# Kernel optimization log

Measured on AMD Instinct MI355X. Metric: run time of the kernel, lower is better.

The kernel has to match this reference:

```python
import jax, jax.numpy as jnp
import numpy as np

N, E, D = 10000, 640000, 128
H1, H2, OUT = 256, 256, 64
EPS = 1e-5

def _layernorm(h, g, b):
    m = jnp.mean(h, axis=-1, keepdims=True)
    v = jnp.mean((h - m) ** 2, axis=-1, keepdims=True)
    return (h - m) * jax.lax.rsqrt(v + EPS) * g + b

def setup_inputs() -> dict:
    key = jax.random.key(0)
    ks = jax.random.split(key, 20)
    def lin(k, fan_in, fan_out):
        bound = 1.0 / np.sqrt(fan_in)
        kw, kb = jax.random.split(k)
        W = jax.random.uniform(kw, (fan_in, fan_out), jnp.float32, -bound, bound)
        b = jax.random.uniform(kb, (fan_out,), jnp.float32, -bound, bound)
        return W, b
    pool_w, pool_b = lin(ks[0], D, D)
    w1, b1 = lin(ks[1], D, H1)
    w2, b2 = lin(ks[2], H1, H2)
    mu_w, mu_b = lin(ks[3], H2, OUT)
    lv_w, lv_b = lin(ks[4], H2, OUT)
    return {
        "x": jax.random.normal(ks[5], (N, D), jnp.float32),
        "edge_index": jax.random.randint(ks[6], (2, E), 0, N, jnp.int32),
        "edge_strength": jax.random.uniform(ks[7], (E,), jnp.float32),
        "ewmc": jnp.float32(0.5),
        "pool_w": pool_w, "pool_b": pool_b,
        "lnp_g": jnp.ones((D,), jnp.float32), "lnp_b": jnp.zeros((D,), jnp.float32),
        "w1": w1, "b1": b1,
        "ln1_g": jnp.ones((H1,), jnp.float32), "ln1_b": jnp.zeros((H1,), jnp.float32),
        "w2": w2, "b2": b2,
        "ln2_g": jnp.ones((H2,), jnp.float32), "ln2_b": jnp.zeros((H2,), jnp.float32),
        "mu_w": mu_w, "mu_b": mu_b,
        "lv_w": lv_w, "lv_b": lv_b,
    }

def reference(x, edge_index, edge_strength, ewmc, pool_w, pool_b, lnp_g, lnp_b,
              w1, b1, ln1_g, ln1_b, w2, b2, ln2_g, ln2_b, mu_w, mu_b, lv_w, lv_b):
    src, dst = edge_index[0], edge_index[1]
    coef = jax.nn.softplus(ewmc)
    # [E, D] gather + edge scaling
    msgs = x[src] * (1.0 + coef * edge_strength[:, None])
    pooled = jax.nn.relu(_layernorm(msgs @ pool_w + pool_b, lnp_g, lnp_b))
    # segment max by dst; torch_scatter fills empty segments with 0 and pooled >= 0
    agg = jax.ops.segment_max(pooled, dst, num_segments=x.shape[0])
    agg = jnp.maximum(agg, 0.0)
    h = jax.nn.relu(_layernorm(agg @ w1 + b1, ln1_g, ln1_b))
    h = jax.nn.relu(_layernorm(h @ w2 + b2, ln2_g, ln2_b))
    mu = h @ mu_w + mu_b
    logvar = h @ lv_w + lv_b
    std = jnp.exp(0.5 * logvar)
    return (mu, std)
```

## Files before the change

### kernel.cpp

```cpp
#include <hip/hip_runtime.h>
#include <math.h>

#define D_DIM   128
#define H1_DIM  256
#define H2_DIM  256
#define OUT_DIM 64
#define LN_EPS  1e-5f
#define NSHARD  4
#define AGGP_STRIDE 2048

typedef __attribute__((ext_vector_type(8))) short bf16x8;
typedef __attribute__((ext_vector_type(4))) float f32x4;

__device__ __forceinline__ unsigned short bf16rne(float v) {
    unsigned int b = __float_as_uint(v);
    return (unsigned short)((b + 0x7FFFu + ((b >> 16) & 1u)) >> 16);
}

union BFPack { unsigned int u[4]; bf16x8 v; };

__global__ __launch_bounds__(512) void k_pool(
        const float* __restrict__ x, const float* __restrict__ pw,
        const float* __restrict__ pb,
        unsigned short* __restrict__ y, float4* __restrict__ stat4,
        const int* __restrict__ ei, int* __restrict__ cnt, int E, int epb,
        const float* __restrict__ w1, const float* __restrict__ w2,
        const float* __restrict__ muw, const float* __restrict__ lvw,
        short* __restrict__ wp1, short* __restrict__ wp2,
        short* __restrict__ wpH) {
    __shared__ __align__(16) short aPack[4 * 64 * 8];
    __shared__ unsigned short yLds[16][128];
    __shared__ float sPart[16][8][3];
    const int tid  = threadIdx.x;
    const int w    = tid >> 6;
    const int lane = tid & 63;
    const int gq   = lane >> 4;
    const int c16  = lane & 15;
    const int row0 = blockIdx.x * 16;

    bf16x8 bfrag[4];
    {
        const int col = w * 16 + c16;
        const int kbase = gq * 8;
#pragma unroll
        for (int kt = 0; kt < 4; ++kt) {
            int k0 = kt * 32 + kbase;
            BFPack t;
#pragma unroll
            for (int jj = 0; jj < 4; ++jj) {
                float a = pw[(k0 + 2 * jj) * D_DIM + col];
                float b = pw[(k0 + 2 * jj + 1) * D_DIM + col];
                t.u[jj] = (unsigned int)bf16rne(a) | ((unsigned int)bf16rne(b) << 16);
            }
            bfrag[kt] = t.v;
        }
    }
    {
        int ebeg = blockIdx.x * epb;
        int eend = ebeg + epb; if (eend > E) eend = E;
        for (int e = ebeg + tid; e < eend; e += 512)
            atomicAdd(&cnt[ei[E + e] * NSHARD + (e & (NSHARD - 1))], 1);
    }
    {
        int r  = tid >> 5;
        int k0 = (tid & 31) * 4;
        float4 v = *(const float4*)&x[(size_t)(row0 + r) * D_DIM + k0];
        int kt = k0 >> 5, sub = (k0 >> 3) & 3, j = k0 & 7;
        int lp = r | (sub << 4);
        unsigned int u0 = (unsigned int)bf16rne(v.x) | ((unsigned int)bf16rne(v.y) << 16);
        unsigned int u1 = (unsigned int)bf16rne(v.z) | ((unsigned int)bf16rne(v.w) << 16);
        *(uint2*)&aPack[kt * 512 + lp * 8 + j] = make_uint2(u0, u1);
    }
    __syncthreads();

    f32x4 A = {0.f, 0.f, 0.f, 0.f};
#pragma unroll
    for (int kt = 0; kt < 4; ++kt) {
        bf16x8 av = *(bf16x8*)&aPack[(kt * 64 + lane) * 8];
        A = __builtin_amdgcn_mfma_f32_16x16x32_bf16(av, bfrag[kt], A, 0, 0, 0);
    }

    {
        float pbf = pb[w * 16 + c16];
#pragma unroll
        for (int r = 0; r < 4; ++r) {
            unsigned short h = bf16rne(A[r]);
            yLds[gq * 4 + r][w * 16 + c16] = h;
            float hf = __uint_as_float((unsigned int)h << 16);
            float s1 = hf, s2 = hf * hf, s3 = hf * pbf;
#pragma unroll
            for (int m = 1; m < 16; m <<= 1) {
                s1 += __shfl_xor(s1, m, 64);
                s2 += __shfl_xor(s2, m, 64);
                s3 += __shfl_xor(s3, m, 64);
            }
            if (c16 == 0) {
                sPart[gq * 4 + r][w][0] = s1;
                sPart[gq * 4 + r][w][1] = s2;
                sPart[gq * 4 + r][w][2] = s3;
            }
        }
    }
    __syncthreads();
    {
        int idx = tid * 4;
        int r = idx >> 7, c = idx & 127;
        *(uint2*)&y[(size_t)(row0 + r) * D_DIM + c] = *(const uint2*)&yLds[r][c];
    }
    if (tid < 16) {
        float t1 = 0.f, t2 = 0.f, t3 = 0.f;
#pragma unroll
        for (int ww = 0; ww < 8; ++ww) {
            t1 += sPart[tid][ww][0]; t2 += sPart[tid][ww][1]; t3 += sPart[tid][ww][2];
        }
        stat4[row0 + tid] = make_float4(t1 * (1.f / 128.f), t2 * (1.f / 128.f),
                                        t3 * (1.f / 128.f), 0.f);
    }
    if (blockIdx.x < 32) {
        int i = blockIdx.x * 512 + tid;
        const float* W; int Ndim, kt, ln, col; short* dst;
        if (i < 4096) {
            int q = i >> 6; ln = i & 63; kt = q & 3; int ct = q >> 2;
            W = w1; Ndim = H1_DIM; col = ct * 16 + (ln & 15); dst = wp1 + i * 8;
        } else if (i < 12288) {
            int i2 = i - 4096; int q = i2 >> 6; ln = i2 & 63; kt = q & 7; int ct = q >> 3;
            W = w2; Ndim = H2_DIM; col = ct * 16 + (ln & 15); dst = wp2 + i2 * 8;
        } else {
            int i3 = i - 12288; int q = i3 >> 6; ln = i3 & 63; kt = q & 7; int ct = q >> 3;
            Ndim = OUT_DIM; dst = wpH + i3 * 8;
            if (ct < 4) { W = muw; col = ct * 16 + (ln & 15); }
            else        { W = lvw; col = (ct - 4) * 16 + (ln & 15); }
        }
        int k0 = kt * 32 + (ln >> 4) * 8;
        unsigned int u[4];
#pragma unroll
        for (int jj = 0; jj < 4; ++jj) {
            float a = W[(k0 + 2 * jj) * Ndim + col];
            float b = W[(k0 + 2 * jj + 1) * Ndim + col];
            u[jj] = (unsigned int)bf16rne(a) | ((unsigned int)bf16rne(b) << 16);
        }
        *(uint4*)dst = make_uint4(u[0], u[1], u[2], u[3]);
    }
}

__global__ __launch_bounds__(1024) void k_scanA(
        const int* __restrict__ cnt, int* __restrict__ offs,
        int* __restrict__ bsum, int N4) {
    __shared__ int part[1024];
    const int t = threadIdx.x;
    const int idx = blockIdx.x * 1024 + t;
    int v = (idx < N4) ? cnt[idx] : 0;
    part[t] = v;
    __syncthreads();
    for (int off = 1; off < 1024; off <<= 1) {
        int n = (t >= off) ? part[t - off] : 0;
        __syncthreads();
        part[t] += n;
        __syncthreads();
    }
    if (idx < N4) offs[idx] = part[t] - v;
    if (t == 1023) bsum[blockIdx.x] = part[t];
}

__global__ __launch_bounds__(64) void k_scanB(
        const int* __restrict__ bsum, int* __restrict__ bbase,
        int* __restrict__ offs, float* __restrict__ consts,
        const float* __restrict__ ewmc, const float* __restrict__ pb,
        int nblk, int N4) {
    const int l = threadIdx.x;
    {
        float v0 = pb[l], v1 = pb[l + 64];
        float s1 = v0 + v1, s2 = v0 * v0 + v1 * v1;
#pragma unroll
        for (int off = 1; off < 64; off <<= 1) {
            s1 += __shfl_xor(s1, off, 64);
            s2 += __shfl_xor(s2, off, 64);
        }
        if (l == 0) {
            float xw = ewmc[0];
            consts[0] = (xw > 30.f) ? xw : log1pf(expf(xw));
            consts[1] = s1 * (1.f / 128.f);
            consts[2] = s2 * (1.f / 128.f);
        }
    }
    int val = (l < nblk) ? bsum[l] : 0;
    int orig = val;
#pragma unroll
    for (int off = 1; off < 64; off <<= 1) {
        int n = __shfl_up(val, off, 64);
        if (l >= off) val += n;
    }
    if (l < nblk) bbase[l] = val - orig;
    if (l == nblk - 1) offs[N4] = val;
}

__global__ __launch_bounds__(1024) void k_scanC(
        int* __restrict__ offs, int* __restrict__ head,
        const int* __restrict__ bbase, int N4) {
    int idx = blockIdx.x * 1024 + threadIdx.x;
    if (idx < N4) {
        int o = offs[idx] + bbase[blockIdx.x];
        offs[idx] = o;
        head[idx] = o;
    }
}

__global__ __launch_bounds__(256) void k_scatter(
        const int* __restrict__ ei, const float* __restrict__ es,
        const float* __restrict__ consts, const float4* __restrict__ stat4,
        int* __restrict__ head, float4* __restrict__ pairs, int E) {
    const float coef = consts[0], mpb = consts[1], mpb2 = consts[2];
    const int tid = threadIdx.x;
    const int e0 = blockIdx.x * 2048 + tid;
    int srcv[8], dstv[8]; float sv[8]; float4 st[8]; int pos[8]; bool ok[8];
#pragma unroll
    for (int u = 0; u < 8; ++u) {
        int e = e0 + u * 256;
        ok[u] = (e < E);
        if (ok[u]) { srcv[u] = ei[e]; dstv[u] = ei[E + e]; sv[u] = es[e]; }
    }
#pragma unroll
    for (int u = 0; u < 8; ++u) if (ok[u]) st[u] = stat4[srcv[u]];
#pragma unroll
    for (int u = 0; u < 8; ++u) if (ok[u]) {
        int e = e0 + u * 256;
        pos[u] = atomicAdd(&head[dstv[u] * NSHARD + (e & (NSHARD - 1))], 1);
    }
#pragma unroll
    for (int u = 0; u < 8; ++u) if (ok[u]) {
        float s = fmaf(coef, sv[u], 1.0f);
        float m   = fmaf(s, st[u].x, mpb);
        float et2 = fmaf(s * s, st[u].y, fmaf(2.f * s, st[u].z, mpb2));
        float inv = rsqrtf(et2 - m * m + LN_EPS);
        pairs[pos[u]] = make_float4(__int_as_float(srcv[u]), s, m, inv);
    }
}

#define GPROC(P, YB)                                                          \
    {                                                                         \
        float s = (P).y, m = (P).z, inv = (P).w;                              \
        float y0 = __uint_as_float((YB).x << 16);                             \
        float y1 = __uint_as_float((YB).x & 0xFFFF0000u);                     \
        float y2 = __uint_as_float((YB).y << 16);                             \
        float y3 = __uint_as_float((YB).y & 0xFFFF0000u);                     \
        float y4 = __uint_as_float((YB).z << 16);                             \
        float y5 = __uint_as_float((YB).z & 0xFFFF0000u);                     \
        float y6 = __uint_as_float((YB).w << 16);                             \
        float y7 = __uint_as_float((YB).w & 0xFFFF0000u);                     \
        mxA.x = fmaxf(mxA.x, fmaf(fmaf(s, y0, pbA.x) - m, inv * gA.x, bA.x)); \
        mxA.y = fmaxf(mxA.y, fmaf(fmaf(s, y1, pbA.y) - m, inv * gA.y, bA.y)); \
        mxA.z = fmaxf(mxA.z, fmaf(fmaf(s, y2, pbA.z) - m, inv * gA.z, bA.z)); \
        mxA.w = fmaxf(mxA.w, fmaf(fmaf(s, y3, pbA.w) - m, inv * gA.w, bA.w)); \
        mxB.x = fmaxf(mxB.x, fmaf(fmaf(s, y4, pbB.x) - m, inv * gB.x, bB.x)); \
        mxB.y = fmaxf(mxB.y, fmaf(fmaf(s, y5, pbB.y) - m, inv * gB.y, bB.y)); \
        mxB.z = fmaxf(mxB.z, fmaf(fmaf(s, y6, pbB.z) - m, inv * gB.z, bB.z)); \
        mxB.w = fmaxf(mxB.w, fmaf(fmaf(s, y7, pbB.w) - m, inv * gB.w, bB.w)); \
    }

__global__ __launch_bounds__(256) void k_gather(
        const float4* __restrict__ pairs, const int* __restrict__ offs,
        const unsigned short* __restrict__ y, const float* __restrict__ pb,
        const float* __restrict__ g, const float* __restrict__ b,
        unsigned short* __restrict__ aggP, int N) {
    const int node = blockIdx.x * 4 + (threadIdx.x >> 6);
    if (node >= N) return;
    const int lane = threadIdx.x & 63;
    const int sub  = lane >> 4;
    const int q    = lane & 15;
    const int d0   = q * 8;
    const float4 pbA = *(const float4*)&pb[d0], pbB = *(const float4*)&pb[d0 + 4];
    const float4 gA  = *(const float4*)&g[d0],  gB  = *(const float4*)&g[d0 + 4];
    const float4 bA  = *(const float4*)&b[d0],  bB  = *(const float4*)&b[d0 + 4];
    float4 mxA = make_float4(-INFINITY, -INFINITY, -INFINITY, -INFINITY);
    float4 mxB = mxA;
    int j = offs[node * NSHARD];
    const int end = offs[node * NSHARD + NSHARD];
    for (; j + 12 <= end; j += 12) {
        float4 p[3]; uint4 yb[3];
#pragma unroll
        for (int u = 0; u < 3; ++u) p[u] = pairs[j + 4 * u + sub];
#pragma unroll
        for (int u = 0; u < 3; ++u)
            yb[u] = *(const uint4*)&y[(size_t)__float_as_int(p[u].x) * D_DIM + d0];
#pragma unroll
        for (int u = 0; u < 3; ++u) GPROC(p[u], yb[u]);
    }
    for (; j + 4 <= end; j += 4) {
        float4 p = pairs[j + sub];
        uint4 yb = *(const uint4*)&y[(size_t)__float_as_int(p.x) * D_DIM + d0];
        GPROC(p, yb);
    }
    if (j < end) {
        int rem = end - j;
        float4 p = pairs[j + (sub < rem ? sub : 0)];
        uint4 yb = *(const uint4*)&y[(size_t)__float_as_int(p.x) * D_DIM + d0];
        GPROC(p, yb);
    }
    mxA.x = fmaxf(mxA.x, __shfl_xor(mxA.x, 16, 64));
    mxA.y = fmaxf(mxA.y, __shfl_xor(mxA.y, 16, 64));
    mxA.z = fmaxf(mxA.z, __shfl_xor(mxA.z, 16, 64));
    mxA.w = fmaxf(mxA.w, __shfl_xor(mxA.w, 16, 64));
    mxB.x = fmaxf(mxB.x, __shfl_xor(mxB.x, 16, 64));
    mxB.y = fmaxf(mxB.y, __shfl_xor(mxB.y, 16, 64));
    mxB.z = fmaxf(mxB.z, __shfl_xor(mxB.z, 16, 64));
    mxB.w = fmaxf(mxB.w, __shfl_xor(mxB.w, 16, 64));
    mxA.x = fmaxf(mxA.x, __shfl_xor(mxA.x, 32, 64));
    mxA.y = fmaxf(mxA.y, __shfl_xor(mxA.y, 32, 64));
    mxA.z = fmaxf(mxA.z, __shfl_xor(mxA.z, 32, 64));
    mxA.w = fmaxf(mxA.w, __shfl_xor(mxA.w, 32, 64));
    mxB.x = fmaxf(mxB.x, __shfl_xor(mxB.x, 32, 64));
    mxB.y = fmaxf(mxB.y, __shfl_xor(mxB.y, 32, 64));
    mxB.z = fmaxf(mxB.z, __shfl_xor(mxB.z, 32, 64));
    mxB.w = fmaxf(mxB.w, __shfl_xor(mxB.w, 32, 64));
    if (sub == 0) {
        unsigned int u0 = (unsigned int)bf16rne(fmaxf(mxA.x, 0.f))
                        | ((unsigned int)bf16rne(fmaxf(mxA.y, 0.f)) << 16);
        unsigned int u1 = (unsigned int)bf16rne(fmaxf(mxA.z, 0.f))
                        | ((unsigned int)bf16rne(fmaxf(mxA.w, 0.f)) << 16);
        unsigned int u2 = (unsigned int)bf16rne(fmaxf(mxB.x, 0.f))
                        | ((unsigned int)bf16rne(fmaxf(mxB.y, 0.f)) << 16);
        unsigned int u3 = (unsigned int)bf16rne(fmaxf(mxB.z, 0.f))
                        | ((unsigned int)bf16rne(fmaxf(mxB.w, 0.f)) << 16);
        int kt = q >> 2, sfr = q & 3, lp = (node & 15) | (sfr << 4);
        *(uint4*)&aggP[(size_t)(node >> 4) * AGGP_STRIDE + kt * 512 + lp * 8] =
            make_uint4(u0, u1, u2, u3);
    }
}

__global__ __launch_bounds__(512) void k_mlp(
        const unsigned short* __restrict__ aggP,
        const short* __restrict__ wp1, const short* __restrict__ wp2,
        const short* __restrict__ wpH,
        const float* __restrict__ b1, const float* __restrict__ g1,
        const float* __restrict__ bb1,
        const float* __restrict__ b2, const float* __restrict__ g2,
        const float* __restrict__ bb2,
        const float* __restrict__ mub, const float* __restrict__ lvb,
        float* __restrict__ out, int N) {
    __shared__ __align__(16) short aPack[8 * 64 * 8];
    __shared__ float sPart[16][8][2];
    __shared__ float sM[16], sI[16];
    const int tid  = threadIdx.x;
    const int w    = tid >> 6;
    const int lane = tid & 63;
    const int gq   = lane >> 4;
    const int c16  = lane & 15;
    const int row0 = blockIdx.x * 16;
    const unsigned short* aG = aggP + (size_t)blockIdx.x * AGGP_STRIDE;

    const int ct0 = 2 * w, ct1 = 2 * w + 1;
    f32x4 A0 = {0.f, 0.f, 0.f, 0.f}, A1 = {0.f, 0.f, 0.f, 0.f};

#pragma unroll
    for (int kt = 0; kt < 4; ++kt) {
        bf16x8 av = *(const bf16x8*)&aG[(kt * 64 + lane) * 8];
        bf16x8 bv0 = *(const bf16x8*)&wp1[((ct0 * 4 + kt) * 64 + lane) * 8];
        bf16x8 bv1 = *(const bf16x8*)&wp1[((ct1 * 4 + kt) * 64 + lane) * 8];
        A0 = __builtin_amdgcn_mfma_f32_16x16x32_bf16(av, bv0, A0, 0, 0, 0);
        A1 = __builtin_amdgcn_mfma_f32_16x16x32_bf16(av, bv1, A1, 0, 0, 0);
    }
    {
        int col0 = ct0 * 16 + c16, col1 = ct1 * 16 + c16;
        float bias0 = b1[col0], bias1 = b1[col1];
        float v0[4], v1[4];
#pragma unroll
        for (int r = 0; r < 4; ++r) {
            v0[r] = A0[r] + bias0; v1[r] = A1[r] + bias1;
            float s1 = v0[r] + v1[r];
            float s2 = v0[r] * v0[r] + v1[r] * v1[r];
#pragma unroll
            for (int m = 1; m < 16; m <<= 1) {
                s1 += __shfl_xor(s1, m, 64);
                s2 += __shfl_xor(s2, m, 64);
            }
            if (c16 == 0) { sPart[gq * 4 + r][w][0] = s1; sPart[gq * 4 + r][w][1] = s2; }
        }
        __syncthreads();
        if (tid < 16) {
            float t1 = 0.f, t2 = 0.f;
#pragma unroll
            for (int ww = 0; ww < 8; ++ww) { t1 += sPart[tid][ww][0]; t2 += sPart[tid][ww][1]; }
            float m = t1 * (1.f / 256.f);
            sM[tid] = m;
            sI[tid] = rsqrtf(t2 * (1.f / 256.f) - m * m + LN_EPS);
        }
        __syncthreads();
        float gc0 = g1[col0], bc0 = bb1[col0];
        float gc1 = g1[col1], bc1 = bb1[col1];
#pragma unroll
        for (int r = 0; r < 4; ++r) {
            int row = gq * 4 + r;
            float m = sM[row], inv = sI[row];
            float h0 = fmaxf(fmaf((v0[r] - m) * inv, gc0, bc0), 0.f);
            float h1 = fmaxf(fmaf((v1[r] - m) * inv, gc1, bc1), 0.f);
            aPack[(col0 >> 5) * 512 + (row | (((col0 >> 3) & 3) << 4)) * 8 + (col0 & 7)] = (short)bf16rne(h0);
            aPack[(col1 >> 5) * 512 + (row | (((col1 >> 3) & 3) << 4)) * 8 + (col1 & 7)] = (short)bf16rne(h1);
        }
    }
    __syncthreads();

    A0 = (f32x4){0.f, 0.f, 0.f, 0.f}; A1 = (f32x4){0.f, 0.f, 0.f, 0.f};
#pragma unroll
    for (int kt = 0; kt < 8; ++kt) {
        bf16x8 av = *(bf16x8*)&aPack[(kt * 64 + lane) * 8];
        bf16x8 bv0 = *(const bf16x8*)&wp2[((ct0 * 8 + kt) * 64 + lane) * 8];
        bf16x8 bv1 = *(const bf16x8*)&wp2[((ct1 * 8 + kt) * 64 + lane) * 8];
        A0 = __builtin_amdgcn_mfma_f32_16x16x32_bf16(av, bv0, A0, 0, 0, 0);
        A1 = __builtin_amdgcn_mfma_f32_16x16x32_bf16(av, bv1, A1, 0, 0, 0);
    }
    {
        int col0 = ct0 * 16 + c16, col1 = ct1 * 16 + c16;
        float bias0 = b2[col0], bias1 = b2[col1];
        float v0[4], v1[4];
#pragma unroll
        for (int r = 0; r < 4; ++r) {
            v0[r] = A0[r] + bias0; v1[r] = A1[r] + bias1;
            float s1 = v0[r] + v1[r];
            float s2 = v0[r] * v0[r] + v1[r] * v1[r];
#pragma unroll
            for (int m = 1; m < 16; m <<= 1) {
                s1 += __shfl_xor(s1, m, 64);
                s2 += __shfl_xor(s2, m, 64);
            }
            if (c16 == 0) { sPart[gq * 4 + r][w][0] = s1; sPart[gq * 4 + r][w][1] = s2; }
        }
        __syncthreads();
        if (tid < 16) {
            float t1 = 0.f, t2 = 0.f;
#pragma unroll
            for (int ww = 0; ww < 8; ++ww) { t1 += sPart[tid][ww][0]; t2 += sPart[tid][ww][1]; }
            float m = t1 * (1.f / 256.f);
            sM[tid] = m;
            sI[tid] = rsqrtf(t2 * (1.f / 256.f) - m * m + LN_EPS);
        }
        __syncthreads();
        float gc0 = g2[col0], bc0 = bb2[col0];
        float gc1 = g2[col1], bc1 = bb2[col1];
#pragma unroll
        for (int r = 0; r < 4; ++r) {
            int row = gq * 4 + r;
            float m = sM[row], inv = sI[row];
            float h0 = fmaxf(fmaf((v0[r] - m) * inv, gc0, bc0), 0.f);
            float h1 = fmaxf(fmaf((v1[r] - m) * inv, gc1, bc1), 0.f);
            aPack[(col0 >> 5) * 512 + (row | (((col0 >> 3) & 3) << 4)) * 8 + (col0 & 7)] = (short)bf16rne(h0);
            aPack[(col1 >> 5) * 512 + (row | (((col1 >> 3) & 3) << 4)) * 8 + (col1 & 7)] = (short)bf16rne(h1);
        }
    }
    __syncthreads();

    {
        f32x4 H = {0.f, 0.f, 0.f, 0.f};
#pragma unroll
        for (int kt = 0; kt < 8; ++kt) {
            bf16x8 av = *(bf16x8*)&aPack[(kt * 64 + lane) * 8];
            bf16x8 bv = *(const bf16x8*)&wpH[((w * 8 + kt) * 64 + lane) * 8];
            H = __builtin_amdgcn_mfma_f32_16x16x32_bf16(av, bv, H, 0, 0, 0);
        }
        int colh = (w & 3) * 16 + c16;
        if (w < 4) {
            float bias = mub[colh];
#pragma unroll
            for (int r = 0; r < 4; ++r)
                out[(size_t)(row0 + gq * 4 + r) * OUT_DIM + colh] = H[r] + bias;
        } else {
            float bias = lvb[colh];
#pragma unroll
            for (int r = 0; r < 4; ++r)
                out[(size_t)N * OUT_DIM + (size_t)(row0 + gq * 4 + r) * OUT_DIM + colh] =
                    expf(0.5f * (H[r] + bias));
        }
    }
}

extern "C" void kernel_launch(void* const* d_in, const int* in_sizes, int n_in,
                              void* d_out, int out_size, void* d_ws, size_t ws_size,
                              hipStream_t stream) {
    const float* x      = (const float*)d_in[0];
    const int*   ei     = (const int*)  d_in[1];
    const float* es     = (const float*)d_in[2];
    const float* ewmc   = (const float*)d_in[3];
    const float* pool_w = (const float*)d_in[4];
    const float* pool_b = (const float*)d_in[5];
    const float* lnp_g  = (const float*)d_in[6];
    const float* lnp_b  = (const float*)d_in[7];
    const float* w1     = (const float*)d_in[8];
    const float* b1     = (const float*)d_in[9];
    const float* ln1_g  = (const float*)d_in[10];
    const float* ln1_b  = (const float*)d_in[11];
    const float* w2     = (const float*)d_in[12];
    const float* b2     = (const float*)d_in[13];
    const float* ln2_g  = (const float*)d_in[14];
    const float* ln2_b  = (const float*)d_in[15];
    const float* mu_w   = (const float*)d_in[16];
    const float* mu_b   = (const float*)d_in[17];
    const float* lv_w   = (const float*)d_in[18];
    const float* lv_b   = (const float*)d_in[19];

    const int N  = in_sizes[0] / D_DIM;
    const int E  = in_sizes[2];
    const int N4 = N * NSHARD;
    const int nblkScan = (N4 + 1023) / 1024;

    float*  ws     = (float*)d_ws;
    float*  consts = ws;
    float4* stat4  = (float4*)(ws + 16);
    unsigned short* y    = (unsigned short*)(ws + 16 + 4 * (size_t)N);
    unsigned short* aggP = y + (size_t)N * D_DIM;
    size_t  w      = 16 + 4 * (size_t)N + (size_t)N * D_DIM;
    int*    cnt    = (int*)(ws + w); w += N4;
    int*    offs   = (int*)(ws + w); w += N4 + 1;
    int*    head   = (int*)(ws + w); w += N4;
    int*    bsum   = (int*)(ws + w); w += 64;
    int*    bbase  = (int*)(ws + w); w += 64;
    w = (w + 3) & ~(size_t)3;
    short*  wp1    = (short*)(ws + w); w += 16384;
    short*  wp2    = (short*)(ws + w); w += 32768;
    short*  wpH    = (short*)(ws + w); w += 16384;
    float4* pairs  = (float4*)(ws + w);

    const int nbPool = N / 16;
    const int epb    = (E + nbPool - 1) / nbPool;

    hipMemsetAsync(cnt, 0, (size_t)N4 * sizeof(int), stream);
    k_pool<<<nbPool, 512, 0, stream>>>(x, pool_w, pool_b, y, stat4, ei, cnt, E,
                                       epb, w1, w2, mu_w, lv_w, wp1, wp2, wpH);
    k_scanA<<<nblkScan, 1024, 0, stream>>>(cnt, offs, bsum, N4);
    k_scanB<<<1, 64, 0, stream>>>(bsum, bbase, offs, consts, ewmc, pool_b,
                                  nblkScan, N4);
    k_scanC<<<nblkScan, 1024, 0, stream>>>(offs, head, bbase, N4);
    k_scatter<<<(E + 2047) / 2048, 256, 0, stream>>>(ei, es, consts, stat4,
                                                     head, pairs, E);
    k_gather<<<(N + 3) / 4, 256, 0, stream>>>(pairs, offs, y,
                                              pool_b, lnp_g, lnp_b, aggP, N);
    k_mlp<<<N / 16, 512, 0, stream>>>(aggP, wp1, wp2, wpH,
                                      b1, ln1_g, ln1_b,
                                      b2, ln2_g, ln2_b,
                                      mu_b, lv_b, (float*)d_out, N);
}
```

Baseline: 116.5 us.

## Fold scan fix-up kernels into scatter and gather via per-block base recompute

Removes the k_scanB and k_scanC launches. Each scatter and gather block now rebuilds the 64-entry block-base prefix in shared memory from bsum and adds it to the local offsets on the fly. The scatter atomics now run on a zeroed head0 counter array, cleared by the enlarged memset, instead of a copied head. Scatter edges per block drop from 8 to 4 per thread, and the gather unroll grows from 3 to 4. This saves two launches and a pass over the offsets, at the cost of a redundant small prefix scan in every block plus an extra offsL load per edge.

```diff
diff --git a/kernel.cpp b/kernel.cpp
--- a/kernel.cpp
+++ b/kernel.cpp
@@ -144,8 +144,25 @@
 }
 
 __global__ __launch_bounds__(1024) void k_scanA(
-        const int* __restrict__ cnt, int* __restrict__ offs,
-        int* __restrict__ bsum, int N4) {
+        const int* __restrict__ cnt, int* __restrict__ offsL,
+        int* __restrict__ bsum, float* __restrict__ consts,
+        const float* __restrict__ ewmc, const float* __restrict__ pb, int N4) {
+    if (blockIdx.x == 0 && threadIdx.x < 64) {
+        const int l = threadIdx.x;
+        float v0 = pb[l], v1 = pb[l + 64];
+        float s1 = v0 + v1, s2 = v0 * v0 + v1 * v1;
+#pragma unroll
+        for (int off = 1; off < 64; off <<= 1) {
+            s1 += __shfl_xor(s1, off, 64);
+            s2 += __shfl_xor(s2, off, 64);
+        }
+        if (l == 0) {
+            float xw = ewmc[0];
+            consts[0] = (xw > 30.f) ? xw : log1pf(expf(xw));
+            consts[1] = s1 * (1.f / 128.f);
+            consts[2] = s2 * (1.f / 128.f);
+        }
+    }
     __shared__ int part[1024];
     const int t = threadIdx.x;
     const int idx = blockIdx.x * 1024 + t;
@@ -158,81 +175,66 @@
         part[t] += n;
         __syncthreads();
     }
-    if (idx < N4) offs[idx] = part[t] - v;
+    if (idx < N4) offsL[idx] = part[t] - v;
     if (t == 1023) bsum[blockIdx.x] = part[t];
 }
 
-__global__ __launch_bounds__(64) void k_scanB(
-        const int* __restrict__ bsum, int* __restrict__ bbase,
-        int* __restrict__ offs, float* __restrict__ consts,
-        const float* __restrict__ ewmc, const float* __restrict__ pb,
-        int nblk, int N4) {
-    const int l = threadIdx.x;
-    {
-        float v0 = pb[l], v1 = pb[l + 64];
-        float s1 = v0 + v1, s2 = v0 * v0 + v1 * v1;
+__device__ __forceinline__ void build_bb(const int* __restrict__ bsum,
+                                         int* bbL, int* totalL,
+                                         int tid, int nblk) {
+    if (tid < 64) {
+        int v = (tid < nblk) ? bsum[tid] : 0;
+        int val = v;
 #pragma unroll
         for (int off = 1; off < 64; off <<= 1) {
-            s1 += __shfl_xor(s1, off, 64);
-            s2 += __shfl_xor(s2, off, 64);
-        }
-        if (l == 0) {
-            float xw = ewmc[0];
-            consts[0] = (xw > 30.f) ? xw : log1pf(expf(xw));
-            consts[1] = s1 * (1.f / 128.f);
-            consts[2] = s2 * (1.f / 128.f);
-        }
-    }
-    int val = (l < nblk) ? bsum[l] : 0;
-    int orig = val;
-#pragma unroll
-    for (int off = 1; off < 64; off <<= 1) {
-        int n = __shfl_up(val, off, 64);
-        if (l >= off) val += n;
-    }
-    if (l < nblk) bbase[l] = val - orig;
-    if (l == nblk - 1) offs[N4] = val;
-}
-
-__global__ __launch_bounds__(1024) void k_scanC(
-        int* __restrict__ offs, int* __restrict__ head,
-        const int* __restrict__ bbase, int N4) {
-    int idx = blockIdx.x * 1024 + threadIdx.x;
-    if (idx < N4) {
-        int o = offs[idx] + bbase[blockIdx.x];
-        offs[idx] = o;
-        head[idx] = o;
+            int n = __shfl_up(val, off, 64);
+            if (tid >= off) val += n;
+        }
+        if (tid < nblk) bbL[tid] = val - v;
+        if (tid == nblk - 1) *totalL = val;
     }
 }
 
 __global__ __launch_bounds__(256) void k_scatter(
         const int* __restrict__ ei, const float* __restrict__ es,
         const float* __restrict__ consts, const float4* __restrict__ stat4,
-        int* __restrict__ head, float4* __restrict__ pairs, int E) {
+        int* __restrict__ head0, const int* __restrict__ offsL,
+        const int* __restrict__ bsum, float4* __restrict__ pairs,
+        int E, int nblk) {
+    __shared__ int bbL[64];
+    __shared__ int totalL;
+    const int tid = threadIdx.x;
+    build_bb(bsum, bbL, &totalL, tid, nblk);
+    __syncthreads();
     const float coef = consts[0], mpb = consts[1], mpb2 = consts[2];
-    const int tid = threadIdx.x;
-    const int e0 = blockIdx.x * 2048 + tid;
-    int srcv[8], dstv[8]; float sv[8]; float4 st[8]; int pos[8]; bool ok[8];
-#pragma unroll
-    for (int u = 0; u < 8; ++u) {
+    const int e0 = blockIdx.x * 1024 + tid;
+    int srcv[4], idxv[4]; float sv[4]; float4 st[4]; int base[4], pos[4];
+    bool ok[4];
+#pragma unroll
+    for (int u = 0; u < 4; ++u) {
         int e = e0 + u * 256;
         ok[u] = (e < E);
-        if (ok[u]) { srcv[u] = ei[e]; dstv[u] = ei[E + e]; sv[u] = es[e]; }
-    }
-#pragma unroll
-    for (int u = 0; u < 8; ++u) if (ok[u]) st[u] = stat4[srcv[u]];
-#pragma unroll
-    for (int u = 0; u < 8; ++u) if (ok[u]) {
-        int e = e0 + u * 256;
-        pos[u] = atomicAdd(&head[dstv[u] * NSHARD + (e & (NSHARD - 1))], 1);
-    }
-#pragma unroll
-    for (int u = 0; u < 8; ++u) if (ok[u]) {
+        if (ok[u]) {
+            srcv[u] = ei[e];
+            idxv[u] = ei[E + e] * NSHARD + (e & (NSHARD - 1));
+            sv[u] = es[e];
+        }
+    }
+#pragma unroll
+    for (int u = 0; u < 4; ++u) if (ok[u]) {
+        st[u] = stat4[srcv[u]];
+        base[u] = offsL[idxv[u]] + bbL[idxv[u] >> 10];
+    }
+#pragma unroll
+    for (int u = 0; u < 4; ++u) if (ok[u])
+        pos[u] = atomicAdd(&head0[idxv[u]], 1);
+#pragma unroll
+    for (int u = 0; u < 4; ++u) if (ok[u]) {
         float s = fmaf(coef, sv[u], 1.0f);
         float m   = fmaf(s, st[u].x, mpb);
         float et2 = fmaf(s * s, st[u].y, fmaf(2.f * s, st[u].z, mpb2));
         float inv = rsqrtf(et2 - m * m + LN_EPS);
-        pairs[pos[u]] = make_float4(__int_as_float(srcv[u]), s, m, inv);
+        pairs[base[u] + pos[u]] = make_float4(__int_as_float(srcv[u]), s, m, inv);
     }
 }
 
@@ -258,13 +260,19 @@
     }
 
 __global__ __launch_bounds__(256) void k_gather(
-        const float4* __restrict__ pairs, const int* __restrict__ offs,
+        const float4* __restrict__ pairs, const int* __restrict__ offsL,
+        const int* __restrict__ bsum,
         const unsigned short* __restrict__ y, const float* __restrict__ pb,
         const float* __restrict__ g, const float* __restrict__ b,
-        unsigned short* __restrict__ aggP, int N) {
-    const int node = blockIdx.x * 4 + (threadIdx.x >> 6);
+        unsigned short* __restrict__ aggP, int N, int N4, int nblk) {
+    __shared__ int bbL[64];
+    __shared__ int totalL;
+    const int tid = threadIdx.x;
+    build_bb(bsum, bbL, &totalL, tid, nblk);
+    __syncthreads();
+    const int node = blockIdx.x * 4 + (tid >> 6);
     if (node >= N) return;
-    const int lane = threadIdx.x & 63;
+    const int lane = tid & 63;
     const int sub  = lane >> 4;
     const int q    = lane & 15;
     const int d0   = q * 8;
@@ -273,17 +281,19 @@
     const float4 bA  = *(const float4*)&b[d0],  bB  = *(const float4*)&b[d0 + 4];
     float4 mxA = make_float4(-INFINITY, -INFINITY, -INFINITY, -INFINITY);
     float4 mxB = mxA;
-    int j = offs[node * NSHARD];
-    const int end = offs[node * NSHARD + NSHARD];
-    for (; j + 12 <= end; j += 12) {
-        float4 p[3]; uint4 yb[3];
-#pragma unroll
-        for (int u = 0; u < 3; ++u) p[u] = pairs[j + 4 * u + sub];
-#pragma unroll
-        for (int u = 0; u < 3; ++u)
+    const int idx0 = node * NSHARD;
+    const int idxe = idx0 + NSHARD;
+    int j = offsL[idx0] + bbL[idx0 >> 10];
+    const int end = (idxe < N4) ? (offsL[idxe] + bbL[idxe >> 10]) : totalL;
+    for (; j + 16 <= end; j += 16) {
+        float4 p[4]; uint4 yb[4];
+#pragma unroll
+        for (int u = 0; u < 4; ++u) p[u] = pairs[j + 4 * u + sub];
+#pragma unroll
+        for (int u = 0; u < 4; ++u)
             yb[u] = *(const uint4*)&y[(size_t)__float_as_int(p[u].x) * D_DIM + d0];
 #pragma unroll
-        for (int u = 0; u < 3; ++u) GPROC(p[u], yb[u]);
+        for (int u = 0; u < 4; ++u) GPROC(p[u], yb[u]);
     }
     for (; j + 4 <= end; j += 4) {
         float4 p = pairs[j + sub];
@@ -508,10 +518,9 @@
     unsigned short* aggP = y + (size_t)N * D_DIM;
     size_t  w      = 16 + 4 * (size_t)N + (size_t)N * D_DIM;
     int*    cnt    = (int*)(ws + w); w += N4;
-    int*    offs   = (int*)(ws + w); w += N4 + 1;
-    int*    head   = (int*)(ws + w); w += N4;
+    int*    head0  = (int*)(ws + w); w += N4;
+    int*    offsL  = (int*)(ws + w); w += N4;
     int*    bsum   = (int*)(ws + w); w += 64;
-    int*    bbase  = (int*)(ws + w); w += 64;
     w = (w + 3) & ~(size_t)3;
     short*  wp1    = (short*)(ws + w); w += 16384;
     short*  wp2    = (short*)(ws + w); w += 32768;
@@ -521,17 +530,17 @@
     const int nbPool = N / 16;
     const int epb    = (E + nbPool - 1) / nbPool;
 
-    hipMemsetAsync(cnt, 0, (size_t)N4 * sizeof(int), stream);
+    hipMemsetAsync(cnt, 0, 2 * (size_t)N4 * sizeof(int), stream);
     k_pool<<<nbPool, 512, 0, stream>>>(x, pool_w, pool_b, y, stat4, ei, cnt, E,
                                        epb, w1, w2, mu_w, lv_w, wp1, wp2, wpH);
-    k_scanA<<<nblkScan, 1024, 0, stream>>>(cnt, offs, bsum, N4);
-    k_scanB<<<1, 64, 0, stream>>>(bsum, bbase, offs, consts, ewmc, pool_b,
-                                  nblkScan, N4);
-    k_scanC<<<nblkScan, 1024, 0, stream>>>(offs, head, bbase, N4);
-    k_scatter<<<(E + 2047) / 2048, 256, 0, stream>>>(ei, es, consts, stat4,
-                                                     head, pairs, E);
-    k_gather<<<(N + 3) / 4, 256, 0, stream>>>(pairs, offs, y,
-                                              pool_b, lnp_g, lnp_b, aggP, N);
+    k_scanA<<<nblkScan, 1024, 0, stream>>>(cnt, offsL, bsum, consts, ewmc,
+                                           pool_b, N4);
+    k_scatter<<<(E + 1023) / 1024, 256, 0, stream>>>(ei, es, consts, stat4,
+                                                     head0, offsL, bsum,
+                                                     pairs, E, nblkScan);
+    k_gather<<<(N + 3) / 4, 256, 0, stream>>>(pairs, offsL, bsum, y,
+                                              pool_b, lnp_g, lnp_b, aggP,
+                                              N, N4, nblkScan);
     k_mlp<<<N / 16, 512, 0, stream>>>(aggP, wp1, wp2, wpH,
                                       b1, ln1_g, ln1_b,
                                       b2, ln2_g, ln2_b,
```

Measured after the change: 118.4 us. Within noise of the previous version (+1.7%).
